# Kernel optimization log

Hardware: AMD Instinct MI355X
Metric: run time of the kernel (lower is better)

Reference implementation:

```python
import jax, jax.numpy as jnp
import numpy as np

D = 128
N_SRC = 50000
N_DST = 50000
E = 640000
NEG_SLOPE = 0.01  # torch LeakyReLU default


def _lrelu(x):
    return jax.nn.leaky_relu(x, NEG_SLOPE)


def setup_inputs() -> dict:
    key = jax.random.key(0)
    ks = jax.random.split(key, 12)
    s = 1.0 / np.sqrt(D)
    return {
        "feat_src": jax.random.normal(ks[0], (N_SRC, D), jnp.float32),
        "feat_dst": jax.random.normal(ks[1], (N_DST, D), jnp.float32),
        "src_idx": jax.random.randint(ks[2], (E,), 0, N_SRC, jnp.int32),
        "dst_idx": jax.random.randint(ks[3], (E,), 0, N_DST, jnp.int32),
        "W_src": jax.random.uniform(ks[4], (D, D), jnp.float32, -s, s),
        "b_src": jnp.zeros((D,), jnp.float32),
        "W_dst": jax.random.uniform(ks[5], (D, D), jnp.float32, -s, s),
        "b_dst": jnp.zeros((D,), jnp.float32),
        "W_a1": jax.random.uniform(ks[6], (D, D), jnp.float32, -s, s),
        "b_a1": jnp.zeros((D,), jnp.float32),
        "W_a2": jax.random.uniform(ks[7], (D, 1), jnp.float32, -s, s),
        "b_a2": jnp.zeros((1,), jnp.float32),
        "W_out": jax.random.uniform(ks[8], (D, D), jnp.float32, -s, s),
        "b_out": jnp.zeros((D,), jnp.float32),
    }


def reference(feat_src, feat_dst, src_idx, dst_idx,
              W_src, b_src, W_dst, b_dst,
              W_a1, b_a1, W_a2, b_a2, W_out, b_out):
    n_dst = feat_dst.shape[0]
    # node projections (dropout is identity in eval mode)
    hs = feat_src @ W_src + b_src            # [n_src, d]
    hd = feat_dst @ W_dst + b_dst            # [n_dst, d]
    # u_add_v: per-edge feature
    e = hs[src_idx] + hd[dst_idx]            # [E, d]
    # attention MLP: LeakyReLU -> Linear -> LeakyReLU -> Linear(d->1)
    s = _lrelu(_lrelu(e) @ W_a1 + b_a1) @ W_a2 + b_a2  # [E, 1]
    s = s[:, 0]
    # edge softmax grouped by destination node (numerically stable)
    m = jax.ops.segment_max(s, dst_idx, num_segments=n_dst)
    ex = jnp.exp(s - m[dst_idx])
    denom = jax.ops.segment_sum(ex, dst_idx, num_segments=n_dst)
    alpha = ex / denom[dst_idx]              # [E]
    # scale messages and scatter-sum to dst nodes
    n_f = jax.ops.segment_sum(alpha[:, None] * e, dst_idx, num_segments=n_dst)
    return _lrelu(n_f @ W_out + b_out)       # [n_dst, d]
```

## Files before the change

### kernel.cpp

```cpp
#include <hip/hip_runtime.h>
#include <math.h>

#define DD 128
#define NEG 0.01f
#define SCHUNK 4096

typedef __attribute__((ext_vector_type(8))) _Float16 half8;
typedef __attribute__((ext_vector_type(4))) float f32x4;

__device__ __forceinline__ float lrelu(float x){ return x > 0.f ? x : NEG * x; }

__device__ __forceinline__ unsigned short h2u(_Float16 h){
    union { _Float16 h; unsigned short u; } v; v.h = h; return v.u;
}
__device__ __forceinline__ _Float16 u2h(unsigned short u){
    union { unsigned short u; _Float16 h; } v; v.u = u; return v.h;
}

__device__ __forceinline__ half8 h8max(half8 x, half8 y){
#if __has_builtin(__builtin_elementwise_max)
    return __builtin_elementwise_max(x, y);
#else
    half8 r;
    #pragma unroll
    for (int i = 0; i < 8; i++) r[i] = x[i] > y[i] ? x[i] : y[i];
    return r;
#endif
}

__global__ void hist_pack(const int* dst, int* deg, int* rank, int E, int nhist,
                          const float* Wa1, const float* Wsrc,
                          const float* Wdst, const float* Wout,
                          unsigned short* wpack){
    const int bid = blockIdx.x;
    if (bid < nhist){
        int i = bid * 256 + threadIdx.x;
        if (i < E) rank[i] = atomicAdd(&deg[dst[i]], 1);
    } else {
        int i = (bid - nhist) * 256 + threadIdx.x;
        if (i >= 4 * 16384) return;
        int seg = i >> 14, t = i & 16383;
        int j = t & 7, lane = (t >> 3) & 63, nt = (t >> 9) & 7, kc = t >> 12;
        int k = kc * 32 + (lane >> 4) * 8 + j;
        int n = nt * 16 + (lane & 15);
        const float* W = (seg == 0) ? Wa1 : (seg == 1) ? Wsrc : (seg == 2) ? Wdst : Wout;
        wpack[i] = h2u((_Float16)W[k * DD + n]);
    }
}

__global__ __launch_bounds__(1024) void scan1(const int* deg, int* part, int n){
    __shared__ int wsum[16];
    const int tid = threadIdx.x;
    const int lane = tid & 63, wid = tid >> 6;
    int i4 = blockIdx.x * SCHUNK + tid * 4;
    int4 v = make_int4(0, 0, 0, 0);
    if (i4 + 3 < n) v = *(const int4*)(deg + i4);
    else {
        if (i4 + 0 < n) v.x = deg[i4 + 0];
        if (i4 + 1 < n) v.y = deg[i4 + 1];
        if (i4 + 2 < n) v.z = deg[i4 + 2];
        if (i4 + 3 < n) v.w = deg[i4 + 3];
    }
    int t = v.x + v.y + v.z + v.w;
    #pragma unroll
    for (int off = 1; off < 64; off <<= 1) t += __shfl_xor(t, off, 64);
    if (lane == 0) wsum[wid] = t;
    __syncthreads();
    if (tid == 0){
        int s = 0;
        #pragma unroll
        for (int j = 0; j < 16; j++) s += wsum[j];
        part[blockIdx.x] = s;
    }
}

__global__ __launch_bounds__(1024) void scan2(const int* deg, const int* part,
        int* row_off, int n, int nchunks){
    __shared__ int wsum[16];
    const int tid = threadIdx.x;
    const int lane = tid & 63, wid = tid >> 6;
    const int b = blockIdx.x;
    int carry = 0;
    for (int j = 0; j < b; j++) carry += part[j];
    int i4 = b * SCHUNK + tid * 4;
    int4 v = make_int4(0, 0, 0, 0);
    if (i4 + 3 < n) v = *(const int4*)(deg + i4);
    else {
        if (i4 + 0 < n) v.x = deg[i4 + 0];
        if (i4 + 1 < n) v.y = deg[i4 + 1];
        if (i4 + 2 < n) v.z = deg[i4 + 2];
        if (i4 + 3 < n) v.w = deg[i4 + 3];
    }
    int tsum = v.x + v.y + v.z + v.w;
    int x = tsum;
    #pragma unroll
    for (int off = 1; off < 64; off <<= 1){
        int t = __shfl_up(x, off, 64);
        if (lane >= off) x += t;
    }
    if (lane == 63) wsum[wid] = x;
    __syncthreads();
    int wprefix = 0;
    #pragma unroll
    for (int j = 0; j < 16; j++) if (j < wid) wprefix += wsum[j];
    int excl = carry + wprefix + (x - tsum);
    if (i4 + 3 < n){
        int4 o;
        o.x = excl; o.y = excl + v.x; o.z = o.y + v.y; o.w = o.z + v.z;
        *(int4*)(row_off + i4) = o;
    } else {
        int a = excl;
        if (i4 + 0 < n){ row_off[i4 + 0] = a; a += v.x; }
        if (i4 + 1 < n){ row_off[i4 + 1] = a; a += v.y; }
        if (i4 + 2 < n){ row_off[i4 + 2] = a; a += v.z; }
        if (i4 + 3 < n){ row_off[i4 + 3] = a; }
    }
    if (b == 0 && tid == 0){
        int tot = 0;
        for (int j = 0; j < nchunks; j++) tot += part[j];
        row_off[n] = tot;
    }
}

__global__ __launch_bounds__(256) void scatter_lin2(
        const int* src, const int* dst, const int* row_off, const int* rank,
        int2* pairs, int E, int nsc,
        const float* X1, const unsigned short* W1, const float* b1,
        unsigned short* Yb1, int n1, int g1,
        const float* X2, const unsigned short* W2, const float* b2,
        unsigned short* Yb2, int n2){
    __shared__ unsigned short sB[16384];
    const int tid = threadIdx.x;
    if (blockIdx.x < nsc){
        int i = blockIdx.x * 256 + tid;
        if (i < E){
            int d = dst[i];
            pairs[row_off[d] + rank[i]] = make_int2(src[i], d);
        }
        return;
    }
    const int lb = blockIdx.x - nsc;
    const int second = (lb >= g1);
    const float* X = second ? X2 : X1;
    const unsigned short* W = second ? W2 : W1;
    const float* b = second ? b2 : b1;
    unsigned short* Yb = second ? Yb2 : Yb1;
    const int nrows = second ? n2 : n1;
    const int bidx = second ? (lb - g1) : lb;
    {
        const uint4* g = (const uint4*)W;
        uint4* l = (uint4*)sB;
        #pragma unroll
        for (int t = 0; t < 8; t++) l[tid + 256 * t] = g[tid + 256 * t];
    }
    const int wave = tid >> 6, lane = tid & 63;
    const int qd = lane >> 4, ln16 = lane & 15;
    const int row0 = bidx * 128 + wave * 32;
    int r0 = row0 + ln16;       if (r0 >= nrows) r0 = nrows - 1;
    int r1 = row0 + 16 + ln16;  if (r1 >= nrows) r1 = nrows - 1;
    f32x4 acc[2][8];
    #pragma unroll
    for (int rt = 0; rt < 2; rt++)
        #pragma unroll
        for (int nt = 0; nt < 8; nt++)
            acc[rt][nt] = (f32x4){0.f, 0.f, 0.f, 0.f};
    __syncthreads();
    #pragma unroll
    for (int kc = 0; kc < 4; kc++){
        const int koff = kc * 32 + qd * 8;
        half8 a[2];
        const float* px[2] = {X + (size_t)r0 * DD + koff, X + (size_t)r1 * DD + koff};
        #pragma unroll
        for (int rt = 0; rt < 2; rt++){
            float4 v0 = *(const float4*)(px[rt]);
            float4 v1 = *(const float4*)(px[rt] + 4);
            a[rt][0] = (_Float16)v0.x; a[rt][1] = (_Float16)v0.y;
            a[rt][2] = (_Float16)v0.z; a[rt][3] = (_Float16)v0.w;
            a[rt][4] = (_Float16)v1.x; a[rt][5] = (_Float16)v1.y;
            a[rt][6] = (_Float16)v1.z; a[rt][7] = (_Float16)v1.w;
        }
        #pragma unroll
        for (int nt = 0; nt < 8; nt++){
            const int fi = (((kc << 3) + nt) << 6 | lane) << 3;
            half8 bw = *(const half8*)&sB[fi];
            acc[0][nt] = __builtin_amdgcn_mfma_f32_16x16x32_f16(a[0], bw, acc[0][nt], 0, 0, 0);
            acc[1][nt] = __builtin_amdgcn_mfma_f32_16x16x32_f16(a[1], bw, acc[1][nt], 0, 0, 0);
        }
    }
    #pragma unroll
    for (int nt = 0; nt < 8; nt++){
        const int col = nt * 16 + ln16;
        const float bv = b[col];
        #pragma unroll
        for (int rt = 0; rt < 2; rt++){
            #pragma unroll
            for (int r = 0; r < 4; r++){
                int row = row0 + rt * 16 + qd * 4 + r;
                if (row < nrows){
                    float y = acc[rt][nt][r] + bv;
                    Yb[(size_t)row * DD + col] = h2u((_Float16)y);
                }
            }
        }
    }
}

__global__ __launch_bounds__(256) void lin_mfma(const float* X,
        const unsigned short* W, const float* b, float* Y, int nrows){
    __shared__ unsigned short sB[16384];
    const int tid = threadIdx.x;
    {
        const uint4* g = (const uint4*)W;
        uint4* l = (uint4*)sB;
        #pragma unroll
        for (int t = 0; t < 8; t++) l[tid + 256 * t] = g[tid + 256 * t];
    }
    const int wave = tid >> 6, lane = tid & 63;
    const int qd = lane >> 4, ln16 = lane & 15;
    const int row0 = blockIdx.x * 128 + wave * 32;
    int r0 = row0 + ln16;       if (r0 >= nrows) r0 = nrows - 1;
    int r1 = row0 + 16 + ln16;  if (r1 >= nrows) r1 = nrows - 1;
    f32x4 acc[2][8];
    #pragma unroll
    for (int rt = 0; rt < 2; rt++)
        #pragma unroll
        for (int nt = 0; nt < 8; nt++)
            acc[rt][nt] = (f32x4){0.f, 0.f, 0.f, 0.f};
    __syncthreads();
    #pragma unroll
    for (int kc = 0; kc < 4; kc++){
        const int koff = kc * 32 + qd * 8;
        half8 a[2];
        const float* px[2] = {X + (size_t)r0 * DD + koff, X + (size_t)r1 * DD + koff};
        #pragma unroll
        for (int rt = 0; rt < 2; rt++){
            float4 v0 = *(const float4*)(px[rt]);
            float4 v1 = *(const float4*)(px[rt] + 4);
            a[rt][0] = (_Float16)v0.x; a[rt][1] = (_Float16)v0.y;
            a[rt][2] = (_Float16)v0.z; a[rt][3] = (_Float16)v0.w;
            a[rt][4] = (_Float16)v1.x; a[rt][5] = (_Float16)v1.y;
            a[rt][6] = (_Float16)v1.z; a[rt][7] = (_Float16)v1.w;
        }
        #pragma unroll
        for (int nt = 0; nt < 8; nt++){
            const int fi = (((kc << 3) + nt) << 6 | lane) << 3;
            half8 bw = *(const half8*)&sB[fi];
            acc[0][nt] = __builtin_amdgcn_mfma_f32_16x16x32_f16(a[0], bw, acc[0][nt], 0, 0, 0);
            acc[1][nt] = __builtin_amdgcn_mfma_f32_16x16x32_f16(a[1], bw, acc[1][nt], 0, 0, 0);
        }
    }
    #pragma unroll
    for (int nt = 0; nt < 8; nt++){
        const int col = nt * 16 + ln16;
        const float bv = b[col];
        #pragma unroll
        for (int rt = 0; rt < 2; rt++){
            #pragma unroll
            for (int r = 0; r < 4; r++){
                int row = row0 + rt * 16 + qd * 4 + r;
                if (row < nrows){
                    float y = acc[rt][nt][r] + bv;
                    Y[(size_t)row * DD + col] = lrelu(y);
                }
            }
        }
    }
}

__device__ __forceinline__ half8 afrag_from(half8 a, half8 b){
    half8 s = a + b;
    return h8max(s, s * (_Float16)NEG);
}

__global__ __launch_bounds__(512) void edge_score_mfma(
        const unsigned short* hs_h, const unsigned short* hd_h,
        const int2* pairs,
        const unsigned short* wa1p, const float* ba1,
        const float* Wa2, const float* ba2,
        float* s_w, int E){
    __shared__ unsigned short sB[16384];
    const int tid = threadIdx.x;
    {
        const uint4* g = (const uint4*)wa1p;
        uint4* l = (uint4*)sB;
        #pragma unroll
        for (int t = 0; t < 4; t++) l[tid + 512 * t] = g[tid + 512 * t];
    }
    const int wave = tid >> 6, lane = tid & 63;
    const int qd = lane >> 4, ln16 = lane & 15;
    const int e0 = blockIdx.x * 256 + wave * 32;
    float b1v[8], w2v[8];
    #pragma unroll
    for (int nt = 0; nt < 8; nt++){
        b1v[nt] = ba1[nt * 16 + ln16];
        w2v[nt] = Wa2[nt * 16 + ln16];
    }
    __syncthreads();
    for (int rt = 0; rt < 2; rt++){
        int eid = e0 + rt * 16 + ln16;
        if (eid >= E) eid = E - 1;
        const int2 pp = pairs[eid];
        f32x4 acc[8];
        #pragma unroll
        for (int nt = 0; nt < 8; nt++)
            acc[nt] = (f32x4){b1v[nt], b1v[nt], b1v[nt], b1v[nt]};
        #pragma unroll
        for (int kc = 0; kc < 4; kc++){
            const int koff = kc * 32 + qd * 8;
            half8 af = afrag_from(*(const half8*)(hs_h + (size_t)pp.x * DD + koff),
                                  *(const half8*)(hd_h + (size_t)pp.y * DD + koff));
            #pragma unroll
            for (int nt = 0; nt < 8; nt++){
                half8 bf = *(const half8*)&sB[(((kc << 3) + nt) << 6 | lane) << 3];
                acc[nt] = __builtin_amdgcn_mfma_f32_16x16x32_f16(af, bf, acc[nt], 0, 0, 0);
            }
        }
        float p[4] = {0.f, 0.f, 0.f, 0.f};
        #pragma unroll
        for (int nt = 0; nt < 8; nt++)
            #pragma unroll
            for (int r = 0; r < 4; r++){
                float z = acc[nt][r];
                z = fmaxf(z, NEG * z);
                p[r] += z * w2v[nt];
            }
        #pragma unroll
        for (int r = 0; r < 4; r++){
            float v = p[r];
            #pragma unroll
            for (int off = 1; off < 16; off <<= 1) v += __shfl_xor(v, off, 64);
            p[r] = __expf(v);
        }
        if (ln16 == 0){
            int row = e0 + rt * 16 + qd * 4;
            #pragma unroll
            for (int r = 0; r < 4; r++)
                if (row + r < E) s_w[row + r] = p[r];
        }
    }
}

__global__ __launch_bounds__(256) void agg_softmax(const unsigned short* hs_h,
        const unsigned short* hd_h, const int* row_off, const int2* pairs,
        const float* s_w, float* nf, int n_dst){
    const int w = (blockIdx.x * blockDim.x + threadIdx.x) >> 6;
    const int lane = threadIdx.x & 63;
    if (w >= n_dst) return;
    const int beg = row_off[w], end = row_off[w + 1];
    const int hf = lane >> 5, l32 = lane & 31;
    float4 acc = make_float4(0.f, 0.f, 0.f, 0.f);
    float sa = 0.f;
    int e = beg;
    for (; e + 7 < end; e += 8){
        int rows[4]; float wv[4]; ushort4 uv[4];
        #pragma unroll
        for (int j = 0; j < 4; j++){
            int ee = e + 2 * j + hf;
            rows[j] = pairs[ee].x;
            wv[j] = s_w[ee];
        }
        #pragma unroll
        for (int j = 0; j < 4; j++)
            uv[j] = *(const ushort4*)(hs_h + (size_t)rows[j] * DD + l32 * 4);
        #pragma unroll
        for (int j = 0; j < 4; j++){
            acc.x += wv[j] * (float)u2h(uv[j].x);
            acc.y += wv[j] * (float)u2h(uv[j].y);
            acc.z += wv[j] * (float)u2h(uv[j].z);
            acc.w += wv[j] * (float)u2h(uv[j].w);
            sa += wv[j];
        }
    }
    for (; e < end; e += 4){
        int ee0 = e + hf;          int ee1 = e + 2 + hf;
        int ec0 = ee0 < end ? ee0 : end - 1;
        int ec1 = ee1 < end ? ee1 : end - 1;
        int r0 = pairs[ec0].x, r1 = pairs[ec1].x;
        float wv0 = (ee0 < end) ? s_w[ec0] : 0.f;
        float wv1 = (ee1 < end) ? s_w[ec1] : 0.f;
        ushort4 u0 = *(const ushort4*)(hs_h + (size_t)r0 * DD + l32 * 4);
        ushort4 u1 = *(const ushort4*)(hs_h + (size_t)r1 * DD + l32 * 4);
        acc.x += wv0 * (float)u2h(u0.x) + wv1 * (float)u2h(u1.x);
        acc.y += wv0 * (float)u2h(u0.y) + wv1 * (float)u2h(u1.y);
        acc.z += wv0 * (float)u2h(u0.z) + wv1 * (float)u2h(u1.z);
        acc.w += wv0 * (float)u2h(u0.w) + wv1 * (float)u2h(u1.w);
        sa += wv0 + wv1;
    }
    acc.x += __shfl_xor(acc.x, 32, 64);
    acc.y += __shfl_xor(acc.y, 32, 64);
    acc.z += __shfl_xor(acc.z, 32, 64);
    acc.w += __shfl_xor(acc.w, 32, 64);
    sa    += __shfl_xor(sa, 32, 64);
    const float inv = (end > beg) ? 1.f / sa : 0.f;
    if (hf == 0){
        ushort4 hu = *(const ushort4*)(hd_h + (size_t)w * DD + l32 * 4);
        const float gx = (end > beg) ? 1.f : 0.f;
        float4 out;
        out.x = acc.x * inv + gx * (float)u2h(hu.x);
        out.y = acc.y * inv + gx * (float)u2h(hu.y);
        out.z = acc.z * inv + gx * (float)u2h(hu.z);
        out.w = acc.w * inv + gx * (float)u2h(hu.w);
        *(float4*)(nf + (size_t)w * DD + l32 * 4) = out;
    }
}

extern "C" void kernel_launch(void* const* d_in, const int* in_sizes, int n_in,
                              void* d_out, int out_size, void* d_ws, size_t ws_size,
                              hipStream_t stream){
    const float* feat_src = (const float*)d_in[0];
    const float* feat_dst = (const float*)d_in[1];
    const int*   src_idx  = (const int*)d_in[2];
    const int*   dst_idx  = (const int*)d_in[3];
    const float* W_src = (const float*)d_in[4];
    const float* b_src = (const float*)d_in[5];
    const float* W_dst = (const float*)d_in[6];
    const float* b_dst = (const float*)d_in[7];
    const float* W_a1  = (const float*)d_in[8];
    const float* b_a1  = (const float*)d_in[9];
    const float* W_a2  = (const float*)d_in[10];
    const float* b_a2  = (const float*)d_in[11];
    const float* W_out = (const float*)d_in[12];
    const float* b_out = (const float*)d_in[13];
    const int n_src = in_sizes[0] / DD;
    const int n_dst = in_sizes[1] / DD;
    const int E = in_sizes[2];
    const int nchunks = (n_dst + SCHUNK - 1) / SCHUNK;

    char* p = (char*)d_ws;
    unsigned short* hs_h = (unsigned short*)p;  p += (size_t)n_src * DD * 2;
    unsigned short* hd_h = (unsigned short*)p;  p += (size_t)n_dst * DD * 2;
    unsigned short* wpack = (unsigned short*)p; p += 4 * 16384 * 2;
    float* s_w = (float*)p;                     p += (size_t)E * 4;
    int2* pairs = (int2*)p;                     p += (size_t)E * 8;
    int* rank = (int*)p;                        p += (size_t)E * 4;
    int* deg = (int*)p;                         p += (size_t)n_dst * 4;
    int* part = (int*)p;                        p += 64 * 4;
    int* row_off = (int*)p;                     p += ((size_t)n_dst + 1) * 4;
    float* nf = (float*)d_out;

    const unsigned short* wa1p = wpack;
    const unsigned short* wsrc = wpack + 1 * 16384;
    const unsigned short* wdst = wpack + 2 * 16384;
    const unsigned short* wout = wpack + 3 * 16384;

    hipMemsetAsync(deg, 0, (size_t)n_dst * 4, stream);
    const int nhist = (E + 255) / 256;
    const int npack = (4 * 16384 + 255) / 256;
    hist_pack<<<nhist + npack, 256, 0, stream>>>(dst_idx, deg, rank, E, nhist,
                                                 W_a1, W_src, W_dst, W_out, wpack);
    scan1<<<nchunks, 1024, 0, stream>>>(deg, part, n_dst);
    scan2<<<nchunks, 1024, 0, stream>>>(deg, part, row_off, n_dst, nchunks);
    const int nsc = (E + 255) / 256;
    const int g1 = (n_src + 127) / 128;
    const int g2 = (n_dst + 127) / 128;
    scatter_lin2<<<nsc + g1 + g2, 256, 0, stream>>>(src_idx, dst_idx, row_off, rank,
                                                    pairs, E, nsc,
                                                    feat_src, wsrc, b_src, hs_h, n_src, g1,
                                                    feat_dst, wdst, b_dst, hd_h, n_dst);
    edge_score_mfma<<<(E + 255) / 256, 512, 0, stream>>>(hs_h, hd_h, pairs, wa1p, b_a1,
                                                         W_a2, b_a2, s_w, E);
    agg_softmax<<<((size_t)n_dst * 64 + 255) / 256, 256, 0, stream>>>(hs_h, hd_h, row_off,
                                                                      pairs, s_w, nf, n_dst);
    lin_mfma<<<g2, 256, 0, stream>>>(nf, wout, b_out, nf, n_dst);
}
```

Baseline: 272.3 us.

## Fuse edge scoring and softmax aggregation into one per-destination kernel

Replaces the separate edge-score kernel and the softmax-aggregation kernel with a single kernel where each wave handles one destination node. The wave computes the MLP scores for 16 edges at a time with MFMA, stages the edge features in swizzled LDS, and accumulates the exp-weighted sum directly. This drops the intermediate score buffer and the second gather of source rows, and shrinks the pairs array to source indices only. In exchange, low-degree nodes leave MFMA tiles partly empty, and the larger LDS footprint may limit occupancy. The per-node hd term is now folded into each edge feature before aggregation rather than added afterwards.

After: 348.3 us. 1.28x slower.

```diff
diff --git a/kernel.cpp b/kernel.cpp
--- a/kernel.cpp
+++ b/kernel.cpp
@@ -124,7 +124,7 @@
 
 __global__ __launch_bounds__(256) void scatter_lin2(
         const int* src, const int* dst, const int* row_off, const int* rank,
-        int2* pairs, int E, int nsc,
+        int* srcs, int E, int nsc,
         const float* X1, const unsigned short* W1, const float* b1,
         unsigned short* Yb1, int n1, int g1,
         const float* X2, const unsigned short* W2, const float* b2,
@@ -135,7 +135,7 @@
         int i = blockIdx.x * 256 + tid;
         if (i < E){
             int d = dst[i];
-            pairs[row_off[d] + rank[i]] = make_int2(src[i], d);
+            srcs[row_off[d] + rank[i]] = src[i];
         }
         return;
     }
@@ -267,18 +267,13 @@
     }
 }
 
-__device__ __forceinline__ half8 afrag_from(half8 a, half8 b){
-    half8 s = a + b;
-    return h8max(s, s * (_Float16)NEG);
-}
-
-__global__ __launch_bounds__(512) void edge_score_mfma(
+__global__ __launch_bounds__(512, 4) void attn_fused(
         const unsigned short* hs_h, const unsigned short* hd_h,
-        const int2* pairs,
+        const int* row_off, const int* srcs,
         const unsigned short* wa1p, const float* ba1,
-        const float* Wa2, const float* ba2,
-        float* s_w, int E){
+        const float* Wa2, float* nf, int n_dst){
     __shared__ unsigned short sB[16384];
+    __shared__ unsigned short ebuf[8][2048];
     const int tid = threadIdx.x;
     {
         const uint4* g = (const uint4*)wa1p;
@@ -288,7 +283,7 @@
     }
     const int wave = tid >> 6, lane = tid & 63;
     const int qd = lane >> 4, ln16 = lane & 15;
-    const int e0 = blockIdx.x * 256 + wave * 32;
+    const int w = blockIdx.x * 8 + wave;
     float b1v[8], w2v[8];
     #pragma unroll
     for (int nt = 0; nt < 8; nt++){
@@ -296,26 +291,44 @@
         w2v[nt] = Wa2[nt * 16 + ln16];
     }
     __syncthreads();
-    for (int rt = 0; rt < 2; rt++){
-        int eid = e0 + rt * 16 + ln16;
-        if (eid >= E) eid = E - 1;
-        const int2 pp = pairs[eid];
+    if (w >= n_dst) return;
+    const int beg = row_off[w], end = row_off[w + 1];
+    char* eb = (char*)&ebuf[wave][0];
+    half8 hdr[4];
+    #pragma unroll
+    for (int kc = 0; kc < 4; kc++)
+        hdr[kc] = *(const half8*)(hd_h + (size_t)w * DD + kc * 32 + qd * 8);
+    float a0 = 0.f, a1 = 0.f, ssum = 0.f;
+    for (int c = beg; c < end; c += 16){
+        int eid = c + ln16;
+        int ecl = eid < end ? eid : end - 1;
+        int sidx = srcs[ecl];
+        const unsigned short* ps = hs_h + (size_t)sidx * DD;
+        half8 ef[4];
+        #pragma unroll
+        for (int kc = 0; kc < 4; kc++)
+            ef[kc] = *(const half8*)(ps + kc * 32 + qd * 8) + hdr[kc];
+        #pragma unroll
+        for (int kc = 0; kc < 4; kc++){
+            int wb = ln16 * 256 + ((kc * 64 + qd * 16) ^ ((ln16 & 7) << 4));
+            *(half8*)(eb + wb) = ef[kc];
+        }
         f32x4 acc[8];
         #pragma unroll
         for (int nt = 0; nt < 8; nt++)
             acc[nt] = (f32x4){b1v[nt], b1v[nt], b1v[nt], b1v[nt]};
         #pragma unroll
         for (int kc = 0; kc < 4; kc++){
-            const int koff = kc * 32 + qd * 8;
-            half8 af = afrag_from(*(const half8*)(hs_h + (size_t)pp.x * DD + koff),
-                                  *(const half8*)(hd_h + (size_t)pp.y * DD + koff));
+            half8 af = h8max(ef[kc], ef[kc] * (_Float16)NEG);
             #pragma unroll
             for (int nt = 0; nt < 8; nt++){
                 half8 bf = *(const half8*)&sB[(((kc << 3) + nt) << 6 | lane) << 3];
                 acc[nt] = __builtin_amdgcn_mfma_f32_16x16x32_f16(af, bf, acc[nt], 0, 0, 0);
             }
         }
-        float p[4] = {0.f, 0.f, 0.f, 0.f};
+        float p[4];
+        #pragma unroll
+        for (int r = 0; r < 4; r++) p[r] = 0.f;
         #pragma unroll
         for (int nt = 0; nt < 8; nt++)
             #pragma unroll
@@ -329,79 +342,24 @@
             float v = p[r];
             #pragma unroll
             for (int off = 1; off < 16; off <<= 1) v += __shfl_xor(v, off, 64);
-            p[r] = __expf(v);
-        }
-        if (ln16 == 0){
-            int row = e0 + rt * 16 + qd * 4;
-            #pragma unroll
-            for (int r = 0; r < 4; r++)
-                if (row + r < E) s_w[row + r] = p[r];
-        }
-    }
-}
-
-__global__ __launch_bounds__(256) void agg_softmax(const unsigned short* hs_h,
-        const unsigned short* hd_h, const int* row_off, const int2* pairs,
-        const float* s_w, float* nf, int n_dst){
-    const int w = (blockIdx.x * blockDim.x + threadIdx.x) >> 6;
-    const int lane = threadIdx.x & 63;
-    if (w >= n_dst) return;
-    const int beg = row_off[w], end = row_off[w + 1];
-    const int hf = lane >> 5, l32 = lane & 31;
-    float4 acc = make_float4(0.f, 0.f, 0.f, 0.f);
-    float sa = 0.f;
-    int e = beg;
-    for (; e + 7 < end; e += 8){
-        int rows[4]; float wv[4]; ushort4 uv[4];
-        #pragma unroll
-        for (int j = 0; j < 4; j++){
-            int ee = e + 2 * j + hf;
-            rows[j] = pairs[ee].x;
-            wv[j] = s_w[ee];
-        }
-        #pragma unroll
-        for (int j = 0; j < 4; j++)
-            uv[j] = *(const ushort4*)(hs_h + (size_t)rows[j] * DD + l32 * 4);
-        #pragma unroll
-        for (int j = 0; j < 4; j++){
-            acc.x += wv[j] * (float)u2h(uv[j].x);
-            acc.y += wv[j] * (float)u2h(uv[j].y);
-            acc.z += wv[j] * (float)u2h(uv[j].z);
-            acc.w += wv[j] * (float)u2h(uv[j].w);
-            sa += wv[j];
-        }
-    }
-    for (; e < end; e += 4){
-        int ee0 = e + hf;          int ee1 = e + 2 + hf;
-        int ec0 = ee0 < end ? ee0 : end - 1;
-        int ec1 = ee1 < end ? ee1 : end - 1;
-        int r0 = pairs[ec0].x, r1 = pairs[ec1].x;
-        float wv0 = (ee0 < end) ? s_w[ec0] : 0.f;
-        float wv1 = (ee1 < end) ? s_w[ec1] : 0.f;
-        ushort4 u0 = *(const ushort4*)(hs_h + (size_t)r0 * DD + l32 * 4);
-        ushort4 u1 = *(const ushort4*)(hs_h + (size_t)r1 * DD + l32 * 4);
-        acc.x += wv0 * (float)u2h(u0.x) + wv1 * (float)u2h(u1.x);
-        acc.y += wv0 * (float)u2h(u0.y) + wv1 * (float)u2h(u1.y);
-        acc.z += wv0 * (float)u2h(u0.z) + wv1 * (float)u2h(u1.z);
-        acc.w += wv0 * (float)u2h(u0.w) + wv1 * (float)u2h(u1.w);
-        sa += wv0 + wv1;
-    }
-    acc.x += __shfl_xor(acc.x, 32, 64);
-    acc.y += __shfl_xor(acc.y, 32, 64);
-    acc.z += __shfl_xor(acc.z, 32, 64);
-    acc.w += __shfl_xor(acc.w, 32, 64);
-    sa    += __shfl_xor(sa, 32, 64);
-    const float inv = (end > beg) ? 1.f / sa : 0.f;
-    if (hf == 0){
-        ushort4 hu = *(const ushort4*)(hd_h + (size_t)w * DD + l32 * 4);
-        const float gx = (end > beg) ? 1.f : 0.f;
-        float4 out;
-        out.x = acc.x * inv + gx * (float)u2h(hu.x);
-        out.y = acc.y * inv + gx * (float)u2h(hu.y);
-        out.z = acc.z * inv + gx * (float)u2h(hu.z);
-        out.w = acc.w * inv + gx * (float)u2h(hu.w);
-        *(float4*)(nf + (size_t)w * DD + l32 * 4) = out;
-    }
+            p[r] = (c + qd * 4 + r < end) ? __expf(v) : 0.f;
+        }
+        asm volatile("s_waitcnt lgkmcnt(0)" ::: "memory");
+        #pragma unroll
+        for (int s = 0; s < 16; s++){
+            float wv = __shfl(p[s & 3], (s >> 2) << 4, 64);
+            int rb = s * 256 + ((lane * 4) ^ ((s & 7) << 4));
+            ushort2 ev = *(const ushort2*)(eb + rb);
+            a0 += wv * (float)u2h(ev.x);
+            a1 += wv * (float)u2h(ev.y);
+            ssum += wv;
+        }
+    }
+    const float inv = (end > beg) ? 1.f / ssum : 0.f;
+    float2 o;
+    o.x = a0 * inv;
+    o.y = a1 * inv;
+    *(float2*)(nf + (size_t)w * DD + lane * 2) = o;
 }
 
 extern "C" void kernel_launch(void* const* d_in, const int* in_sizes, int n_in,
@@ -430,8 +388,7 @@
     unsigned short* hs_h = (unsigned short*)p;  p += (size_t)n_src * DD * 2;
     unsigned short* hd_h = (unsigned short*)p;  p += (size_t)n_dst * DD * 2;
     unsigned short* wpack = (unsigned short*)p; p += 4 * 16384 * 2;
-    float* s_w = (float*)p;                     p += (size_t)E * 4;
-    int2* pairs = (int2*)p;                     p += (size_t)E * 8;
+    int* srcs = (int*)p;                        p += (size_t)E * 4;
     int* rank = (int*)p;                        p += (size_t)E * 4;
     int* deg = (int*)p;                         p += (size_t)n_dst * 4;
     int* part = (int*)p;                        p += 64 * 4;
@@ -454,12 +411,10 @@
     const int g1 = (n_src + 127) / 128;
     const int g2 = (n_dst + 127) / 128;
     scatter_lin2<<<nsc + g1 + g2, 256, 0, stream>>>(src_idx, dst_idx, row_off, rank,
-                                                    pairs, E, nsc,
+                                                    srcs, E, nsc,
                                                     feat_src, wsrc, b_src, hs_h, n_src, g1,
                                                     feat_dst, wdst, b_dst, hd_h, n_dst);
-    edge_score_mfma<<<(E + 255) / 256, 512, 0, stream>>>(hs_h, hd_h, pairs, wa1p, b_a1,
-                                                         W_a2, b_a2, s_w, E);
-    agg_softmax<<<((size_t)n_dst * 64 + 255) / 256, 256, 0, stream>>>(hs_h, hd_h, row_off,
-                                                                      pairs, s_w, nf, n_dst);
+    attn_fused<<<(n_dst + 7) / 8, 512, 0, stream>>>(hs_h, hd_h, row_off, srcs,
+                                                    wa1p, b_a1, W_a2, nf, n_dst);
     lin_mfma<<<g2, 256, 0, stream>>>(nf, wout, b_out, nf, n_dst);
 }
```

## Fuse softmax aggregation with output linear layer via LDS-staged MFMA

Applied to the files above, without the earlier changes.

Merges the per-destination softmax aggregation and the final W_out linear plus LeakyReLU into one kernel. Each 512-thread block aggregates 8 destination nodes, one per wave, and stages the results as fp16 in a swizzled LDS buffer. Each wave then computes one 16-column tile with MFMA and writes the activated output directly. This removes the fp32 round-trip of the intermediate node features through global memory and one kernel launch. In exchange, every small block reloads the full 32KB W_out into LDS, and half of each 16-row MFMA tile is wasted.

Result: no change. 267.2 us (-1.9%).

```diff
diff --git a/kernel.cpp b/kernel.cpp
--- a/kernel.cpp
+++ b/kernel.cpp
@@ -205,68 +205,6 @@
     }
 }
 
-__global__ __launch_bounds__(256) void lin_mfma(const float* X,
-        const unsigned short* W, const float* b, float* Y, int nrows){
-    __shared__ unsigned short sB[16384];
-    const int tid = threadIdx.x;
-    {
-        const uint4* g = (const uint4*)W;
-        uint4* l = (uint4*)sB;
-        #pragma unroll
-        for (int t = 0; t < 8; t++) l[tid + 256 * t] = g[tid + 256 * t];
-    }
-    const int wave = tid >> 6, lane = tid & 63;
-    const int qd = lane >> 4, ln16 = lane & 15;
-    const int row0 = blockIdx.x * 128 + wave * 32;
-    int r0 = row0 + ln16;       if (r0 >= nrows) r0 = nrows - 1;
-    int r1 = row0 + 16 + ln16;  if (r1 >= nrows) r1 = nrows - 1;
-    f32x4 acc[2][8];
-    #pragma unroll
-    for (int rt = 0; rt < 2; rt++)
-        #pragma unroll
-        for (int nt = 0; nt < 8; nt++)
-            acc[rt][nt] = (f32x4){0.f, 0.f, 0.f, 0.f};
-    __syncthreads();
-    #pragma unroll
-    for (int kc = 0; kc < 4; kc++){
-        const int koff = kc * 32 + qd * 8;
-        half8 a[2];
-        const float* px[2] = {X + (size_t)r0 * DD + koff, X + (size_t)r1 * DD + koff};
-        #pragma unroll
-        for (int rt = 0; rt < 2; rt++){
-            float4 v0 = *(const float4*)(px[rt]);
-            float4 v1 = *(const float4*)(px[rt] + 4);
-            a[rt][0] = (_Float16)v0.x; a[rt][1] = (_Float16)v0.y;
-            a[rt][2] = (_Float16)v0.z; a[rt][3] = (_Float16)v0.w;
-            a[rt][4] = (_Float16)v1.x; a[rt][5] = (_Float16)v1.y;
-            a[rt][6] = (_Float16)v1.z; a[rt][7] = (_Float16)v1.w;
-        }
-        #pragma unroll
-        for (int nt = 0; nt < 8; nt++){
-            const int fi = (((kc << 3) + nt) << 6 | lane) << 3;
-            half8 bw = *(const half8*)&sB[fi];
-            acc[0][nt] = __builtin_amdgcn_mfma_f32_16x16x32_f16(a[0], bw, acc[0][nt], 0, 0, 0);
-            acc[1][nt] = __builtin_amdgcn_mfma_f32_16x16x32_f16(a[1], bw, acc[1][nt], 0, 0, 0);
-        }
-    }
-    #pragma unroll
-    for (int nt = 0; nt < 8; nt++){
-        const int col = nt * 16 + ln16;
-        const float bv = b[col];
-        #pragma unroll
-        for (int rt = 0; rt < 2; rt++){
-            #pragma unroll
-            for (int r = 0; r < 4; r++){
-                int row = row0 + rt * 16 + qd * 4 + r;
-                if (row < nrows){
-                    float y = acc[rt][nt][r] + bv;
-                    Y[(size_t)row * DD + col] = lrelu(y);
-                }
-            }
-        }
-    }
-}
-
 __device__ __forceinline__ half8 afrag_from(half8 a, half8 b){
     half8 s = a + b;
     return h8max(s, s * (_Float16)NEG);
@@ -340,14 +278,25 @@
     }
 }
 
-__global__ __launch_bounds__(256) void agg_softmax(const unsigned short* hs_h,
-        const unsigned short* hd_h, const int* row_off, const int2* pairs,
-        const float* s_w, float* nf, int n_dst){
-    const int w = (blockIdx.x * blockDim.x + threadIdx.x) >> 6;
-    const int lane = threadIdx.x & 63;
-    if (w >= n_dst) return;
-    const int beg = row_off[w], end = row_off[w + 1];
+__global__ __launch_bounds__(512) void agg_lin(
+        const unsigned short* hs_h, const unsigned short* hd_h,
+        const int* row_off, const int2* pairs, const float* s_w,
+        const unsigned short* wout, const float* bout,
+        float* Y, int n_dst){
+    __shared__ unsigned short sB[16384];
+    __shared__ unsigned short rbuf[2048];
+    const int tid = threadIdx.x;
+    {
+        const uint4* g = (const uint4*)wout;
+        uint4* l = (uint4*)sB;
+        #pragma unroll
+        for (int t = 0; t < 4; t++) l[tid + 512 * t] = g[tid + 512 * t];
+    }
+    const int wave = tid >> 6, lane = tid & 63;
+    const int w = blockIdx.x * 8 + wave;
     const int hf = lane >> 5, l32 = lane & 31;
+    int beg = 0, end = 0;
+    if (w < n_dst){ beg = row_off[w]; end = row_off[w + 1]; }
     float4 acc = make_float4(0.f, 0.f, 0.f, 0.f);
     float sa = 0.f;
     int e = beg;
@@ -393,14 +342,43 @@
     sa    += __shfl_xor(sa, 32, 64);
     const float inv = (end > beg) ? 1.f / sa : 0.f;
     if (hf == 0){
-        ushort4 hu = *(const ushort4*)(hd_h + (size_t)w * DD + l32 * 4);
-        const float gx = (end > beg) ? 1.f : 0.f;
-        float4 out;
-        out.x = acc.x * inv + gx * (float)u2h(hu.x);
-        out.y = acc.y * inv + gx * (float)u2h(hu.y);
-        out.z = acc.z * inv + gx * (float)u2h(hu.z);
-        out.w = acc.w * inv + gx * (float)u2h(hu.w);
-        *(float4*)(nf + (size_t)w * DD + l32 * 4) = out;
+        float hx = 0.f, hy = 0.f, hz = 0.f, hw = 0.f;
+        if (end > beg){
+            ushort4 hu = *(const ushort4*)(hd_h + (size_t)w * DD + l32 * 4);
+            hx = (float)u2h(hu.x); hy = (float)u2h(hu.y);
+            hz = (float)u2h(hu.z); hw = (float)u2h(hu.w);
+        }
+        ushort4 hv;
+        hv.x = h2u((_Float16)(acc.x * inv + hx));
+        hv.y = h2u((_Float16)(acc.y * inv + hy));
+        hv.z = h2u((_Float16)(acc.z * inv + hz));
+        hv.w = h2u((_Float16)(acc.w * inv + hw));
+        int wb = wave * 256 + ((l32 * 8) ^ ((wave & 7) << 4));
+        *(ushort4*)((char*)rbuf + wb) = hv;
+    }
+    __syncthreads();
+    {
+        const int nt = wave;
+        const int qd = lane >> 4, ln16 = lane & 15;
+        f32x4 c = (f32x4){0.f, 0.f, 0.f, 0.f};
+        #pragma unroll
+        for (int kc = 0; kc < 4; kc++){
+            int rb = ln16 * 256 + ((kc * 64 + qd * 16) ^ ((ln16 & 7) << 4));
+            half8 af = *(const half8*)((const char*)rbuf + rb);
+            half8 bf = *(const half8*)&sB[(((kc << 3) + nt) << 6 | lane) << 3];
+            c = __builtin_amdgcn_mfma_f32_16x16x32_f16(af, bf, c, 0, 0, 0);
+        }
+        const int col = nt * 16 + ln16;
+        const float bv = bout[col];
+        #pragma unroll
+        for (int r = 0; r < 4; r++){
+            int row = qd * 4 + r;
+            int node = blockIdx.x * 8 + row;
+            if (row < 8 && node < n_dst){
+                float y = c[r] + bv;
+                Y[(size_t)node * DD + col] = lrelu(y);
+            }
+        }
     }
 }
 
@@ -459,7 +437,6 @@
                                                     feat_dst, wdst, b_dst, hd_h, n_dst);
     edge_score_mfma<<<(E + 255) / 256, 512, 0, stream>>>(hs_h, hd_h, pairs, wa1p, b_a1,
                                                          W_a2, b_a2, s_w, E);
-    agg_softmax<<<((size_t)n_dst * 64 + 255) / 256, 256, 0, stream>>>(hs_h, hd_h, row_off,
-                                                                      pairs, s_w, nf, n_dst);
-    lin_mfma<<<g2, 256, 0, stream>>>(nf, wout, b_out, nf, n_dst);
-}
+    agg_lin<<<(n_dst + 7) / 8, 512, 0, stream>>>(hs_h, hd_h, row_off, pairs, s_w,
+                                                 wout, b_out, nf, n_dst);
+}
```
